# Performance work log

Hardware: AMD Instinct MI355X
Metric: run time of the kernel (lower is better)

Reference implementation:

```python
import jax, jax.numpy as jnp
import numpy as np

B, E, F_IN = 8192, 64, 7
D, H = 64, 4           # feature_size, heads
HD = D // H            # features per head


def setup_inputs() -> dict:
    key = jax.random.key(0)
    ks = jax.random.split(key, 14)
    def lin(k, i, o):
        return jax.random.normal(k, (i, o), jnp.float32) * (1.0 / np.sqrt(i))
    return {
        "x": jax.random.normal(ks[0], (B, E, F_IN), jnp.float32),
        # ego embedding MLP (7->64->64, with bias)
        "ego_w0": lin(ks[1], F_IN, D), "ego_b0": jnp.zeros((D,), jnp.float32),
        "ego_w1": lin(ks[2], D, D),    "ego_b1": jnp.zeros((D,), jnp.float32),
        # others embedding MLP (separate weights)
        "oth_w0": lin(ks[3], F_IN, D), "oth_b0": jnp.zeros((D,), jnp.float32),
        "oth_w1": lin(ks[4], D, D),    "oth_b1": jnp.zeros((D,), jnp.float32),
        # attention projections (no bias)
        "Wk": lin(ks[5], D, D), "Wv": lin(ks[6], D, D),
        "Wq": lin(ks[7], D, D), "Wc": lin(ks[8], D, D),
    }


def _mlp(x, w0, b0, w1, b1):
    h = jax.nn.relu(x @ w0 + b0)
    return jax.nn.relu(h @ w1 + b1)


def reference(x, ego_w0, ego_b0, ego_w1, ego_b1,
              oth_w0, oth_b0, oth_w1, oth_b1, Wk, Wv, Wq, Wc):
    b = x.shape[0]
    mask = x[:, :, 0] < 0.5                       # [B, E] absent entities
    ego = _mlp(x[:, 0:1, :], ego_w0, ego_b0, ego_w1, ego_b1)   # [B, 1, D]
    others = _mlp(x[:, 1:, :], oth_w0, oth_b0, oth_w1, oth_b1)  # [B, E-1, D]
    input_all = jnp.concatenate([ego, others], axis=1)          # [B, E, D]

    # project and split heads -> [B, H, E, HD]
    k = (input_all @ Wk).reshape(b, E, H, HD).transpose(0, 2, 1, 3)
    v = (input_all @ Wv).reshape(b, E, H, HD).transpose(0, 2, 1, 3)
    q = (ego @ Wq).reshape(b, 1, H, HD).transpose(0, 2, 1, 3)   # [B, H, 1, HD]

    scores = jnp.einsum('bhqd,bhkd->bhqk', q, k) / np.sqrt(HD)  # [B, H, 1, E]
    scores = jnp.where(mask[:, None, None, :], -1e9, scores)
    p_attn = jax.nn.softmax(scores, axis=-1)
    out = jnp.einsum('bhqk,bhkd->bhqd', p_attn, v)              # [B, H, 1, HD]
    out = out.reshape(b, D)                                      # concat heads
    result = (out @ Wc + ego[:, 0, :]) * 0.5                     # [B, D]
    return result
```

## Files before the change

### kernel.cpp

```cpp
#include <hip/hip_runtime.h>
#include <hip/hip_bf16.h>


typedef __attribute__((ext_vector_type(8))) short short8;
typedef __attribute__((ext_vector_type(4))) short short4b;
typedef __attribute__((ext_vector_type(4))) float f32x4;

#define SY 72

#define LDS_FENCE() asm volatile("s_waitcnt lgkmcnt(0)" ::: "memory")

#define WS_G    0
#define WS_EGW0 16384
#define WS_EGW1 16896
#define WS_WVT  20992
#define WS_WCT  25088
#define WS_W0T  29184
#define WS_W1T  29696

__device__ __forceinline__ short f2bs(float x) {
    __hip_bfloat16 h = __float2bfloat16(x);
    return __builtin_bit_cast(short, h);
}
__device__ __forceinline__ unsigned short f2u(float x) {
    __hip_bfloat16 h = __float2bfloat16(x);
    return __builtin_bit_cast(unsigned short, h);
}
__device__ __forceinline__ short8 ldws8(const unsigned short* p) {
    return *(const short8*)p;
}

__global__ void pack_ws(const float* __restrict__ ego_w0, const float* __restrict__ ego_w1,
                        const float* __restrict__ oth_w0, const float* __restrict__ oth_w1,
                        const float* __restrict__ Wk, const float* __restrict__ Wv,
                        const float* __restrict__ Wq, const float* __restrict__ Wc,
                        unsigned short* __restrict__ ws) {
    const int blk = blockIdx.x, t = threadIdx.x;
    if (blk < 256) {
        const int n = blk, h = n >> 6, f = n & 63, j = t;
        float a = 0.f;
#pragma unroll
        for (int d = 0; d < 16; ++d)
            a = fmaf(Wq[j * 64 + h * 16 + d], Wk[f * 64 + h * 16 + d], a);
        ws[WS_G + n * 64 + j] = f2u(a);
    } else {
        const int n = blk - 256, k = t;
        ws[WS_EGW1 + n * 64 + k] = f2u(ego_w1[k * 64 + n]);
        ws[WS_WVT  + n * 64 + k] = f2u(Wv[k * 64 + n]);
        ws[WS_WCT  + n * 64 + k] = f2u(Wc[k * 64 + n]);
        ws[WS_W1T  + n * 64 + k] = f2u(oth_w1[k * 64 + n]);
        if (k < 8) {
            ws[WS_EGW0 + n * 8 + k] = (k < 7) ? f2u(ego_w0[k * 64 + n]) : 0;
            ws[WS_W0T  + n * 8 + k] = (k < 7) ? f2u(oth_w0[k * 64 + n]) : 0;
        }
    }
}

__global__ __launch_bounds__(64, 2)
void ego_attn_kernel(const float* __restrict__ x,
                     const float* __restrict__ ego_b0, const float* __restrict__ ego_b1,
                     const float* __restrict__ oth_b0, const float* __restrict__ oth_b1,
                     const unsigned short* __restrict__ ws,
                     float* __restrict__ out)
{
    __shared__ __align__(16) short hy[64 * SY];
    __shared__ __align__(16) short chainbuf[4 * SY];
    __shared__ __align__(16) short kqb[16 * SY];
    __shared__ __align__(16) short pa[16 * SY];
    __shared__ __align__(16) short py[16 * SY];
    __shared__ __align__(16) short ob[4 * SY];
    __shared__ __align__(16) float mbuf[4][64];

    const int lane = threadIdx.x;
    const int lg = lane >> 4, ln = lane & 15;
    const int gb = blockIdx.x * 4;

    const short8 z8 = {0, 0, 0, 0, 0, 0, 0, 0};

    short8 w0f[4], w1f[2][4];
#pragma unroll
    for (int ct = 0; ct < 4; ++ct)
        w0f[ct] = (lg == 0) ? ldws8(ws + WS_W0T + (ct * 16 + ln) * 8) : z8;
#pragma unroll
    for (int kc = 0; kc < 2; ++kc)
#pragma unroll
        for (int ct = 0; ct < 4; ++ct)
            w1f[kc][ct] = ldws8(ws + WS_W1T + (ct * 16 + ln) * 64 + kc * 32 + lg * 8);
    float b0v[4], b1v[4], eb0v[4], eb1v[4];
#pragma unroll
    for (int ct = 0; ct < 4; ++ct) {
        b0v[ct]  = oth_b0[ct * 16 + ln];
        b1v[ct]  = oth_b1[ct * 16 + ln];
        eb0v[ct] = ego_b0[ct * 16 + ln];
        eb1v[ct] = ego_b1[ct * 16 + ln];
    }

    short8 xab[4][4];
#pragma unroll
    for (int i = 0; i < 4; ++i) {
        const float* xb = x + (size_t)(gb + i) * 448;
        mbuf[i][lane] = xb[lane * 7];
#pragma unroll
        for (int mt = 0; mt < 4; ++mt) {
            short8 v = z8;
            if (lg == 0) {
                const float* xr = xb + (mt * 16 + ln) * 7;
#pragma unroll
                for (int k = 0; k < 7; ++k) v[k] = f2bs(xr[k]);
            }
            xab[i][mt] = v;
        }
    }

    short8 xea = z8;
    if (lg == 0 && ln < 4) {
        const float* xr = x + (size_t)(gb + ln) * 448;
#pragma unroll
        for (int i = 0; i < 7; ++i) xea[i] = f2bs(xr[i]);
    }
#pragma unroll
    for (int ct = 0; ct < 4; ++ct) {
        const short8 bfr = (lg == 0) ? ldws8(ws + WS_EGW0 + (ct * 16 + ln) * 8) : z8;
        f32x4 c = {eb0v[ct], eb0v[ct], eb0v[ct], eb0v[ct]};
        c = __builtin_amdgcn_mfma_f32_16x16x32_bf16(xea, bfr, c, 0, 0, 0);
        if (lg == 0) {
#pragma unroll
            for (int r = 0; r < 4; ++r)
                chainbuf[r * SY + ct * 16 + ln] = f2bs(fmaxf(c[r], 0.f));
        }
    }
    LDS_FENCE();
    short8 ha[2];
#pragma unroll
    for (int kc = 0; kc < 2; ++kc)
        ha[kc] = *(const short8*)&chainbuf[(ln & 3) * SY + kc * 32 + lg * 8];
    LDS_FENCE();

    float egoR[4][4];
#pragma unroll
    for (int ct = 0; ct < 4; ++ct) {
        f32x4 c = {eb1v[ct], eb1v[ct], eb1v[ct], eb1v[ct]};
#pragma unroll
        for (int kc = 0; kc < 2; ++kc) {
            const short8 bfr = ldws8(ws + WS_EGW1 + (ct * 16 + ln) * 64 + kc * 32 + lg * 8);
            c = __builtin_amdgcn_mfma_f32_16x16x32_bf16(ha[kc], bfr, c, 0, 0, 0);
        }
#pragma unroll
        for (int r = 0; r < 4; ++r) egoR[ct][r] = fmaxf(c[r], 0.f);
    }
    if (lg == 0) {
#pragma unroll
        for (int ct = 0; ct < 4; ++ct)
#pragma unroll
            for (int r = 0; r < 4; ++r)
                chainbuf[r * SY + ct * 16 + ln] = f2bs(egoR[ct][r]);
    }
    LDS_FENCE();
    short8 ea[2];
#pragma unroll
    for (int kc = 0; kc < 2; ++kc)
        ea[kc] = *(const short8*)&chainbuf[(ln & 3) * SY + kc * 32 + lg * 8];

#pragma unroll
    for (int ctg = 0; ctg < 16; ++ctg) {
        f32x4 c = {0.f, 0.f, 0.f, 0.f};
#pragma unroll
        for (int kc = 0; kc < 2; ++kc) {
            const short8 bfr = ldws8(ws + WS_G + (ctg * 16 + ln) * 64 + kc * 32 + lg * 8);
            c = __builtin_amdgcn_mfma_f32_16x16x32_bf16(ea[kc], bfr, c, 0, 0, 0);
        }
        if (lg == 0) {
            const int h = ctg >> 2, fc = (ctg & 3) * 16 + ln;
#pragma unroll
            for (int r = 0; r < 4; ++r)
                kqb[(r * 4 + h) * SY + fc] = f2bs(c[r] * 0.25f);
        }
    }
    LDS_FENCE();

#pragma unroll
    for (int i = 0; i < 4; ++i) {
#pragma unroll
        for (int mt = 0; mt < 4; ++mt)
#pragma unroll
            for (int ct = 0; ct < 4; ++ct) {
                f32x4 c = {b0v[ct], b0v[ct], b0v[ct], b0v[ct]};
                c = __builtin_amdgcn_mfma_f32_16x16x32_bf16(xab[i][mt], w0f[ct], c, 0, 0, 0);
#pragma unroll
                for (int r = 0; r < 4; ++r)
                    hy[(mt * 16 + lg * 4 + r) * SY + ct * 16 + ln] = f2bs(fmaxf(c[r], 0.f));
            }
        LDS_FENCE();
        short8 a2[4][2];
#pragma unroll
        for (int mt = 0; mt < 4; ++mt)
#pragma unroll
            for (int kc = 0; kc < 2; ++kc)
                a2[mt][kc] = *(const short8*)&hy[(mt * 16 + ln) * SY + kc * 32 + lg * 8];
        LDS_FENCE();
#pragma unroll
        for (int ct = 0; ct < 4; ++ct)
#pragma unroll
            for (int mt = 0; mt < 4; ++mt) {
                f32x4 c = {b1v[ct], b1v[ct], b1v[ct], b1v[ct]};
                c = __builtin_amdgcn_mfma_f32_16x16x32_bf16(a2[mt][0], w1f[0][ct], c, 0, 0, 0);
                c = __builtin_amdgcn_mfma_f32_16x16x32_bf16(a2[mt][1], w1f[1][ct], c, 0, 0, 0);
#pragma unroll
                for (int r = 0; r < 4; ++r)
                    hy[(mt * 16 + lg * 4 + r) * SY + ct * 16 + ln] = f2bs(fmaxf(c[r], 0.f));
            }
        if (lg == 0) {
#pragma unroll
            for (int ct = 0; ct < 4; ++ct)
                hy[ct * 16 + ln] = f2bs(egoR[ct][i]);
        }
        LDS_FENCE();
        short8 ya[4][2];
#pragma unroll
        for (int mt = 0; mt < 4; ++mt)
#pragma unroll
            for (int kc = 0; kc < 2; ++kc)
                ya[mt][kc] = *(const short8*)&hy[(mt * 16 + ln) * SY + kc * 32 + lg * 8];
        short8 kb[2];
#pragma unroll
        for (int kc = 0; kc < 2; ++kc)
            kb[kc] = *(const short8*)&kqb[(i * 4 + (ln & 3)) * SY + kc * 32 + lg * 8];

        float sv[16];
        float m = -3e38f;
#pragma unroll
        for (int mt = 0; mt < 4; ++mt) {
            f32x4 c = {0.f, 0.f, 0.f, 0.f};
            c = __builtin_amdgcn_mfma_f32_16x16x32_bf16(ya[mt][0], kb[0], c, 0, 0, 0);
            c = __builtin_amdgcn_mfma_f32_16x16x32_bf16(ya[mt][1], kb[1], c, 0, 0, 0);
            const float4 mk = *(const float4*)&mbuf[i][mt * 16 + lg * 4];
            const float mkv[4] = {mk.x, mk.y, mk.z, mk.w};
#pragma unroll
            for (int r = 0; r < 4; ++r) {
                float s = c[r];
                if (mkv[r] < 0.5f) s = -1e9f;
                sv[mt * 4 + r] = s;
                m = fmaxf(m, s);
            }
        }
        m = fmaxf(m, __shfl_xor(m, 16));
        m = fmaxf(m, __shfl_xor(m, 32));
        float sum = 0.f;
#pragma unroll
        for (int k = 0; k < 16; ++k) { sv[k] = __expf(sv[k] - m); sum += sv[k]; }
        sum += __shfl_xor(sum, 16);
        sum += __shfl_xor(sum, 32);
        const float inv = 1.f / sum;
#pragma unroll
        for (int mt = 0; mt < 4; ++mt) {
            short4b pk;
#pragma unroll
            for (int r = 0; r < 4; ++r) pk[r] = f2bs(sv[mt * 4 + r] * inv);
            *(short4b*)&pa[ln * SY + mt * 16 + lg * 4] = pk;
        }
        LDS_FENCE();
        short8 pf[2];
#pragma unroll
        for (int kc = 0; kc < 2; ++kc)
            pf[kc] = *(const short8*)&pa[ln * SY + kc * 32 + lg * 8];
#pragma unroll
        for (int ct = 0; ct < 4; ++ct) {
            f32x4 c = {0.f, 0.f, 0.f, 0.f};
#pragma unroll
            for (int kc = 0; kc < 2; ++kc) {
                short8 yv;
#pragma unroll
                for (int j = 0; j < 8; ++j)
                    yv[j] = hy[(kc * 32 + lg * 8 + j) * SY + ct * 16 + ln];
                c = __builtin_amdgcn_mfma_f32_16x16x32_bf16(pf[kc], yv, c, 0, 0, 0);
            }
            if (lg == 0) {
#pragma unroll
                for (int r = 0; r < 4; ++r)
                    py[(r * 4 + i) * SY + ct * 16 + ln] = f2bs(c[r]);
            }
        }
        LDS_FENCE();
    }

#pragma unroll
    for (int ct = 0; ct < 4; ++ct) {
        short8 af[2];
#pragma unroll
        for (int kc = 0; kc < 2; ++kc)
            af[kc] = *(const short8*)&py[(ct * 4 + (ln & 3)) * SY + kc * 32 + lg * 8];
        f32x4 c = {0.f, 0.f, 0.f, 0.f};
#pragma unroll
        for (int kc = 0; kc < 2; ++kc) {
            const short8 bfr = ldws8(ws + WS_WVT + (ct * 16 + ln) * 64 + kc * 32 + lg * 8);
            c = __builtin_amdgcn_mfma_f32_16x16x32_bf16(af[kc], bfr, c, 0, 0, 0);
        }
        if (lg == 0) {
#pragma unroll
            for (int r = 0; r < 4; ++r)
                ob[r * SY + ct * 16 + ln] = f2bs(c[r]);
        }
    }
    LDS_FENCE();
    short8 oa[2];
#pragma unroll
    for (int kc = 0; kc < 2; ++kc)
        oa[kc] = *(const short8*)&ob[(ln & 3) * SY + kc * 32 + lg * 8];
#pragma unroll
    for (int ct = 0; ct < 4; ++ct) {
        f32x4 c = {0.f, 0.f, 0.f, 0.f};
#pragma unroll
        for (int kc = 0; kc < 2; ++kc) {
            const short8 bfr = ldws8(ws + WS_WCT + (ct * 16 + ln) * 64 + kc * 32 + lg * 8);
            c = __builtin_amdgcn_mfma_f32_16x16x32_bf16(oa[kc], bfr, c, 0, 0, 0);
        }
        if (lg == 0) {
#pragma unroll
            for (int r = 0; r < 4; ++r)
                out[(size_t)(gb + r) * 64 + ct * 16 + ln] = (c[r] + egoR[ct][r]) * 0.5f;
        }
    }
}

extern "C" void kernel_launch(void* const* d_in, const int* in_sizes, int n_in,
                              void* d_out, int out_size, void* d_ws, size_t ws_size,
                              hipStream_t stream) {
    const float* x      = (const float*)d_in[0];
    const float* ego_w0 = (const float*)d_in[1];
    const float* ego_b0 = (const float*)d_in[2];
    const float* ego_w1 = (const float*)d_in[3];
    const float* ego_b1 = (const float*)d_in[4];
    const float* oth_w0 = (const float*)d_in[5];
    const float* oth_b0 = (const float*)d_in[6];
    const float* oth_w1 = (const float*)d_in[7];
    const float* oth_b1 = (const float*)d_in[8];
    const float* Wk     = (const float*)d_in[9];
    const float* Wv     = (const float*)d_in[10];
    const float* Wq     = (const float*)d_in[11];
    const float* Wc     = (const float*)d_in[12];

    unsigned short* ws = (unsigned short*)d_ws;
    pack_ws<<<320, 64, 0, stream>>>(ego_w0, ego_w1, oth_w0, oth_w1,
                                    Wk, Wv, Wq, Wc, ws);
    ego_attn_kernel<<<2048, 64, 0, stream>>>(
        x, ego_b0, ego_b1, oth_b0, oth_b1, ws, (float*)d_out);
}
```

Before: 122.6 us.

## Halve batch rows per block, shrink LDS and registers to raise occupancy

Each 64-thread block now handles 2 batch rows instead of 4, so the grid doubles to 4096 blocks and launch bounds ask for 4 waves per SIMD. LDS buffers shrink (fewer rows, unpadded stride, chain and output buffers merged), and register-held fragment arrays are replaced by loads from LDS just before use, to cut VGPR pressure. The mask is now kept as per-lane bitmasks in registers instead of an LDS float buffer. In exchange, the 16-row MFMA tiles for the ego and attention steps are less used, and each block repeats weight-fragment loads for half as much work.

```diff
diff --git a/kernel.cpp b/kernel.cpp
--- a/kernel.cpp
+++ b/kernel.cpp
@@ -7,6 +7,7 @@
 typedef __attribute__((ext_vector_type(4))) float f32x4;
 
 #define SY 72
+#define SK 64
 
 #define LDS_FENCE() asm volatile("s_waitcnt lgkmcnt(0)" ::: "memory")
 
@@ -56,7 +57,7 @@
     }
 }
 
-__global__ __launch_bounds__(64, 2)
+__global__ __launch_bounds__(64, 4)
 void ego_attn_kernel(const float* __restrict__ x,
                      const float* __restrict__ ego_b0, const float* __restrict__ ego_b1,
                      const float* __restrict__ oth_b0, const float* __restrict__ oth_b1,
@@ -64,16 +65,14 @@
                      float* __restrict__ out)
 {
     __shared__ __align__(16) short hy[64 * SY];
-    __shared__ __align__(16) short chainbuf[4 * SY];
-    __shared__ __align__(16) short kqb[16 * SY];
-    __shared__ __align__(16) short pa[16 * SY];
-    __shared__ __align__(16) short py[16 * SY];
-    __shared__ __align__(16) short ob[4 * SY];
-    __shared__ __align__(16) float mbuf[4][64];
+    __shared__ __align__(16) short kqb[8 * SK];
+    __shared__ __align__(16) short pa[4 * SK];
+    __shared__ __align__(16) short py[8 * SK];
+    __shared__ __align__(16) short cbob[2 * SK];
 
     const int lane = threadIdx.x;
     const int lg = lane >> 4, ln = lane & 15;
-    const int gb = blockIdx.x * 4;
+    const int gb = blockIdx.x * 2;
 
     const short8 z8 = {0, 0, 0, 0, 0, 0, 0, 0};
 
@@ -95,11 +94,12 @@
         eb1v[ct] = ego_b1[ct * 16 + ln];
     }
 
-    short8 xab[4][4];
-#pragma unroll
-    for (int i = 0; i < 4; ++i) {
+    short8 xab[2][4];
+    unsigned mbits[2];
+#pragma unroll
+    for (int i = 0; i < 2; ++i) {
         const float* xb = x + (size_t)(gb + i) * 448;
-        mbuf[i][lane] = xb[lane * 7];
+        unsigned mb = 0;
 #pragma unroll
         for (int mt = 0; mt < 4; ++mt) {
             short8 v = z8;
@@ -109,14 +109,20 @@
                 for (int k = 0; k < 7; ++k) v[k] = f2bs(xr[k]);
             }
             xab[i][mt] = v;
-        }
+#pragma unroll
+            for (int r = 0; r < 4; ++r) {
+                const float mv = xb[(mt * 16 + lg * 4 + r) * 7];
+                if (mv < 0.5f) mb |= 1u << (mt * 4 + r);
+            }
+        }
+        mbits[i] = mb;
     }
 
     short8 xea = z8;
-    if (lg == 0 && ln < 4) {
+    if (lg == 0 && ln < 2) {
         const float* xr = x + (size_t)(gb + ln) * 448;
 #pragma unroll
-        for (int i = 0; i < 7; ++i) xea[i] = f2bs(xr[i]);
+        for (int k = 0; k < 7; ++k) xea[k] = f2bs(xr[k]);
     }
 #pragma unroll
     for (int ct = 0; ct < 4; ++ct) {
@@ -125,18 +131,18 @@
         c = __builtin_amdgcn_mfma_f32_16x16x32_bf16(xea, bfr, c, 0, 0, 0);
         if (lg == 0) {
 #pragma unroll
-            for (int r = 0; r < 4; ++r)
-                chainbuf[r * SY + ct * 16 + ln] = f2bs(fmaxf(c[r], 0.f));
+            for (int r = 0; r < 2; ++r)
+                cbob[r * SK + ct * 16 + ln] = f2bs(fmaxf(c[r], 0.f));
         }
     }
     LDS_FENCE();
     short8 ha[2];
 #pragma unroll
     for (int kc = 0; kc < 2; ++kc)
-        ha[kc] = *(const short8*)&chainbuf[(ln & 3) * SY + kc * 32 + lg * 8];
-    LDS_FENCE();
-
-    float egoR[4][4];
+        ha[kc] = *(const short8*)&cbob[(ln & 1) * SK + kc * 32 + lg * 8];
+    LDS_FENCE();
+
+    float egoR[4][2];
 #pragma unroll
     for (int ct = 0; ct < 4; ++ct) {
         f32x4 c = {eb1v[ct], eb1v[ct], eb1v[ct], eb1v[ct]};
@@ -146,20 +152,20 @@
             c = __builtin_amdgcn_mfma_f32_16x16x32_bf16(ha[kc], bfr, c, 0, 0, 0);
         }
 #pragma unroll
-        for (int r = 0; r < 4; ++r) egoR[ct][r] = fmaxf(c[r], 0.f);
+        for (int r = 0; r < 2; ++r) egoR[ct][r] = fmaxf(c[r], 0.f);
     }
     if (lg == 0) {
 #pragma unroll
         for (int ct = 0; ct < 4; ++ct)
 #pragma unroll
-            for (int r = 0; r < 4; ++r)
-                chainbuf[r * SY + ct * 16 + ln] = f2bs(egoR[ct][r]);
+            for (int r = 0; r < 2; ++r)
+                cbob[r * SK + ct * 16 + ln] = f2bs(egoR[ct][r]);
     }
     LDS_FENCE();
     short8 ea[2];
 #pragma unroll
     for (int kc = 0; kc < 2; ++kc)
-        ea[kc] = *(const short8*)&chainbuf[(ln & 3) * SY + kc * 32 + lg * 8];
+        ea[kc] = *(const short8*)&cbob[(ln & 1) * SK + kc * 32 + lg * 8];
 
 #pragma unroll
     for (int ctg = 0; ctg < 16; ++ctg) {
@@ -172,14 +178,14 @@
         if (lg == 0) {
             const int h = ctg >> 2, fc = (ctg & 3) * 16 + ln;
 #pragma unroll
-            for (int r = 0; r < 4; ++r)
-                kqb[(r * 4 + h) * SY + fc] = f2bs(c[r] * 0.25f);
-        }
-    }
-    LDS_FENCE();
-
-#pragma unroll
-    for (int i = 0; i < 4; ++i) {
+            for (int r = 0; r < 2; ++r)
+                kqb[(r * 4 + h) * SK + fc] = f2bs(c[r] * 0.25f);
+        }
+    }
+    LDS_FENCE();
+
+#pragma unroll
+    for (int i = 0; i < 2; ++i) {
 #pragma unroll
         for (int mt = 0; mt < 4; ++mt)
 #pragma unroll
@@ -191,54 +197,44 @@
                     hy[(mt * 16 + lg * 4 + r) * SY + ct * 16 + ln] = f2bs(fmaxf(c[r], 0.f));
             }
         LDS_FENCE();
-        short8 a2[4][2];
-#pragma unroll
-        for (int mt = 0; mt < 4; ++mt)
-#pragma unroll
-            for (int kc = 0; kc < 2; ++kc)
-                a2[mt][kc] = *(const short8*)&hy[(mt * 16 + ln) * SY + kc * 32 + lg * 8];
-        LDS_FENCE();
-#pragma unroll
-        for (int ct = 0; ct < 4; ++ct)
-#pragma unroll
-            for (int mt = 0; mt < 4; ++mt) {
+#pragma unroll
+        for (int mt = 0; mt < 4; ++mt) {
+            short8 a20 = *(const short8*)&hy[(mt * 16 + ln) * SY + 0 * 32 + lg * 8];
+            short8 a21 = *(const short8*)&hy[(mt * 16 + ln) * SY + 1 * 32 + lg * 8];
+#pragma unroll
+            for (int ct = 0; ct < 4; ++ct) {
                 f32x4 c = {b1v[ct], b1v[ct], b1v[ct], b1v[ct]};
-                c = __builtin_amdgcn_mfma_f32_16x16x32_bf16(a2[mt][0], w1f[0][ct], c, 0, 0, 0);
-                c = __builtin_amdgcn_mfma_f32_16x16x32_bf16(a2[mt][1], w1f[1][ct], c, 0, 0, 0);
+                c = __builtin_amdgcn_mfma_f32_16x16x32_bf16(a20, w1f[0][ct], c, 0, 0, 0);
+                c = __builtin_amdgcn_mfma_f32_16x16x32_bf16(a21, w1f[1][ct], c, 0, 0, 0);
 #pragma unroll
                 for (int r = 0; r < 4; ++r)
                     hy[(mt * 16 + lg * 4 + r) * SY + ct * 16 + ln] = f2bs(fmaxf(c[r], 0.f));
             }
+        }
         if (lg == 0) {
 #pragma unroll
             for (int ct = 0; ct < 4; ++ct)
                 hy[ct * 16 + ln] = f2bs(egoR[ct][i]);
         }
         LDS_FENCE();
-        short8 ya[4][2];
-#pragma unroll
-        for (int mt = 0; mt < 4; ++mt)
-#pragma unroll
-            for (int kc = 0; kc < 2; ++kc)
-                ya[mt][kc] = *(const short8*)&hy[(mt * 16 + ln) * SY + kc * 32 + lg * 8];
         short8 kb[2];
 #pragma unroll
         for (int kc = 0; kc < 2; ++kc)
-            kb[kc] = *(const short8*)&kqb[(i * 4 + (ln & 3)) * SY + kc * 32 + lg * 8];
+            kb[kc] = *(const short8*)&kqb[(i * 4 + (ln & 3)) * SK + kc * 32 + lg * 8];
 
         float sv[16];
         float m = -3e38f;
 #pragma unroll
         for (int mt = 0; mt < 4; ++mt) {
+            const short8 ya0 = *(const short8*)&hy[(mt * 16 + ln) * SY + 0 * 32 + lg * 8];
+            const short8 ya1 = *(const short8*)&hy[(mt * 16 + ln) * SY + 1 * 32 + lg * 8];
             f32x4 c = {0.f, 0.f, 0.f, 0.f};
-            c = __builtin_amdgcn_mfma_f32_16x16x32_bf16(ya[mt][0], kb[0], c, 0, 0, 0);
-            c = __builtin_amdgcn_mfma_f32_16x16x32_bf16(ya[mt][1], kb[1], c, 0, 0, 0);
-            const float4 mk = *(const float4*)&mbuf[i][mt * 16 + lg * 4];
-            const float mkv[4] = {mk.x, mk.y, mk.z, mk.w};
+            c = __builtin_amdgcn_mfma_f32_16x16x32_bf16(ya0, kb[0], c, 0, 0, 0);
+            c = __builtin_amdgcn_mfma_f32_16x16x32_bf16(ya1, kb[1], c, 0, 0, 0);
 #pragma unroll
             for (int r = 0; r < 4; ++r) {
                 float s = c[r];
-                if (mkv[r] < 0.5f) s = -1e9f;
+                if ((mbits[i] >> (mt * 4 + r)) & 1u) s = -1e9f;
                 sv[mt * 4 + r] = s;
                 m = fmaxf(m, s);
             }
@@ -251,18 +247,20 @@
         sum += __shfl_xor(sum, 16);
         sum += __shfl_xor(sum, 32);
         const float inv = 1.f / sum;
-#pragma unroll
-        for (int mt = 0; mt < 4; ++mt) {
-            short4b pk;
-#pragma unroll
-            for (int r = 0; r < 4; ++r) pk[r] = f2bs(sv[mt * 4 + r] * inv);
-            *(short4b*)&pa[ln * SY + mt * 16 + lg * 4] = pk;
+        if (ln < 4) {
+#pragma unroll
+            for (int mt = 0; mt < 4; ++mt) {
+                short4b pk;
+#pragma unroll
+                for (int r = 0; r < 4; ++r) pk[r] = f2bs(sv[mt * 4 + r] * inv);
+                *(short4b*)&pa[ln * SK + mt * 16 + lg * 4] = pk;
+            }
         }
         LDS_FENCE();
         short8 pf[2];
 #pragma unroll
         for (int kc = 0; kc < 2; ++kc)
-            pf[kc] = *(const short8*)&pa[ln * SY + kc * 32 + lg * 8];
+            pf[kc] = *(const short8*)&pa[(ln & 3) * SK + kc * 32 + lg * 8];
 #pragma unroll
         for (int ct = 0; ct < 4; ++ct) {
             f32x4 c = {0.f, 0.f, 0.f, 0.f};
@@ -277,7 +275,7 @@
             if (lg == 0) {
 #pragma unroll
                 for (int r = 0; r < 4; ++r)
-                    py[(r * 4 + i) * SY + ct * 16 + ln] = f2bs(c[r]);
+                    py[(r * 2 + i) * SK + ct * 16 + ln] = f2bs(c[r]);
             }
         }
         LDS_FENCE();
@@ -288,7 +286,7 @@
         short8 af[2];
 #pragma unroll
         for (int kc = 0; kc < 2; ++kc)
-            af[kc] = *(const short8*)&py[(ct * 4 + (ln & 3)) * SY + kc * 32 + lg * 8];
+            af[kc] = *(const short8*)&py[(ct * 2 + (ln & 1)) * SK + kc * 32 + lg * 8];
         f32x4 c = {0.f, 0.f, 0.f, 0.f};
 #pragma unroll
         for (int kc = 0; kc < 2; ++kc) {
@@ -297,15 +295,15 @@
         }
         if (lg == 0) {
 #pragma unroll
-            for (int r = 0; r < 4; ++r)
-                ob[r * SY + ct * 16 + ln] = f2bs(c[r]);
+            for (int r = 0; r < 2; ++r)
+                cbob[r * SK + ct * 16 + ln] = f2bs(c[r]);
         }
     }
     LDS_FENCE();
     short8 oa[2];
 #pragma unroll
     for (int kc = 0; kc < 2; ++kc)
-        oa[kc] = *(const short8*)&ob[(ln & 3) * SY + kc * 32 + lg * 8];
+        oa[kc] = *(const short8*)&cbob[(ln & 1) * SK + kc * 32 + lg * 8];
 #pragma unroll
     for (int ct = 0; ct < 4; ++ct) {
         f32x4 c = {0.f, 0.f, 0.f, 0.f};
@@ -316,7 +314,7 @@
         }
         if (lg == 0) {
 #pragma unroll
-            for (int r = 0; r < 4; ++r)
+            for (int r = 0; r < 2; ++r)
                 out[(size_t)(gb + r) * 64 + ct * 16 + ln] = (c[r] + egoR[ct][r]) * 0.5f;
         }
     }
@@ -342,6 +340,6 @@
     unsigned short* ws = (unsigned short*)d_ws;
     pack_ws<<<320, 64, 0, stream>>>(ego_w0, ego_w1, oth_w0, oth_w1,
                                     Wk, Wv, Wq, Wc, ws);
-    ego_attn_kernel<<<2048, 64, 0, stream>>>(
+    ego_attn_kernel<<<4096, 64, 0, stream>>>(
         x, ego_b0, ego_b1, oth_b0, oth_b1, ws, (float*)d_out);
 }
```

Result: slower. 181.5 us (+48.0%).

## Swap MFMA operand order for vector LDS stores and XOR-swizzle buffers

Applied to the files above, without the earlier changes.

Swaps the MFMA A/B operands so each lane holds four consecutive output columns. This lets results go to LDS as packed 4-short stores, and the Y buffers use an XOR swizzle in place of padded rows to avoid bank conflicts. A transposed copy of the second MLP layer output (yt) is computed with extra MFMAs, so the P·Y product can read contiguous short8 vectors instead of eight strided scalar loads. The mask is held as a 64-bit ballot instead of an LDS float buffer. In exchange it issues a second set of layer-2 MFMAs and uses more LDS.

```diff
diff --git a/kernel.cpp b/kernel.cpp
--- a/kernel.cpp
+++ b/kernel.cpp
@@ -5,8 +5,6 @@
 typedef __attribute__((ext_vector_type(8))) short short8;
 typedef __attribute__((ext_vector_type(4))) short short4b;
 typedef __attribute__((ext_vector_type(4))) float f32x4;
-
-#define SY 72
 
 #define LDS_FENCE() asm volatile("s_waitcnt lgkmcnt(0)" ::: "memory")
 
@@ -28,6 +26,18 @@
 }
 __device__ __forceinline__ short8 ldws8(const unsigned short* p) {
     return *(const short8*)p;
+}
+__device__ __forceinline__ short4b pk4r(f32x4 c) {
+    short4b p;
+#pragma unroll
+    for (int r = 0; r < 4; ++r) p[r] = f2bs(fmaxf(c[r], 0.f));
+    return p;
+}
+__device__ __forceinline__ short4b pk4(f32x4 c) {
+    short4b p;
+#pragma unroll
+    for (int r = 0; r < 4; ++r) p[r] = f2bs(c[r]);
+    return p;
 }
 
 __global__ void pack_ws(const float* __restrict__ ego_w0, const float* __restrict__ ego_w1,
@@ -63,43 +73,39 @@
                      const unsigned short* __restrict__ ws,
                      float* __restrict__ out)
 {
-    __shared__ __align__(16) short hy[64 * SY];
-    __shared__ __align__(16) short chainbuf[4 * SY];
-    __shared__ __align__(16) short kqb[16 * SY];
-    __shared__ __align__(16) short pa[16 * SY];
-    __shared__ __align__(16) short py[16 * SY];
-    __shared__ __align__(16) short ob[4 * SY];
-    __shared__ __align__(16) float mbuf[4][64];
+    __shared__ __align__(16) short hy[4096];
+    __shared__ __align__(16) short yt[4096];
+    __shared__ __align__(16) short kqb[1024];
+    __shared__ __align__(16) short pyb[1024];
+    __shared__ __align__(16) short s4[256];
 
     const int lane = threadIdx.x;
     const int lg = lane >> 4, ln = lane & 15;
     const int gb = blockIdx.x * 4;
-
     const short8 z8 = {0, 0, 0, 0, 0, 0, 0, 0};
 
     short8 w0f[4], w1f[2][4];
 #pragma unroll
-    for (int ct = 0; ct < 4; ++ct)
-        w0f[ct] = (lg == 0) ? ldws8(ws + WS_W0T + (ct * 16 + ln) * 8) : z8;
+    for (int t = 0; t < 4; ++t)
+        w0f[t] = (lg == 0) ? ldws8(ws + WS_W0T + (t * 16 + ln) * 8) : z8;
 #pragma unroll
     for (int kc = 0; kc < 2; ++kc)
 #pragma unroll
-        for (int ct = 0; ct < 4; ++ct)
-            w1f[kc][ct] = ldws8(ws + WS_W1T + (ct * 16 + ln) * 64 + kc * 32 + lg * 8);
-    float b0v[4], b1v[4], eb0v[4], eb1v[4];
-#pragma unroll
-    for (int ct = 0; ct < 4; ++ct) {
-        b0v[ct]  = oth_b0[ct * 16 + ln];
-        b1v[ct]  = oth_b1[ct * 16 + ln];
-        eb0v[ct] = ego_b0[ct * 16 + ln];
-        eb1v[ct] = ego_b1[ct * 16 + ln];
+        for (int t = 0; t < 4; ++t)
+            w1f[kc][t] = ldws8(ws + WS_W1T + (t * 16 + ln) * 64 + kc * 32 + lg * 8);
+    float b1v[4], eb1v[4];
+#pragma unroll
+    for (int t = 0; t < 4; ++t) {
+        b1v[t]  = oth_b1[t * 16 + ln];
+        eb1v[t] = ego_b1[t * 16 + ln];
     }
 
     short8 xab[4][4];
+    unsigned long long mb64[4];
 #pragma unroll
     for (int i = 0; i < 4; ++i) {
         const float* xb = x + (size_t)(gb + i) * 448;
-        mbuf[i][lane] = xb[lane * 7];
+        mb64[i] = __ballot(xb[lane * 7] < 0.5f);
 #pragma unroll
         for (int mt = 0; mt < 4; ++mt) {
             short8 v = z8;
@@ -111,39 +117,36 @@
             xab[i][mt] = v;
         }
     }
-
     short8 xea = z8;
     if (lg == 0 && ln < 4) {
         const float* xr = x + (size_t)(gb + ln) * 448;
 #pragma unroll
-        for (int i = 0; i < 7; ++i) xea[i] = f2bs(xr[i]);
-    }
-#pragma unroll
-    for (int ct = 0; ct < 4; ++ct) {
-        const short8 bfr = (lg == 0) ? ldws8(ws + WS_EGW0 + (ct * 16 + ln) * 8) : z8;
-        f32x4 c = {eb0v[ct], eb0v[ct], eb0v[ct], eb0v[ct]};
-        c = __builtin_amdgcn_mfma_f32_16x16x32_bf16(xea, bfr, c, 0, 0, 0);
-        if (lg == 0) {
-#pragma unroll
-            for (int r = 0; r < 4; ++r)
-                chainbuf[r * SY + ct * 16 + ln] = f2bs(fmaxf(c[r], 0.f));
-        }
+        for (int k = 0; k < 7; ++k) xea[k] = f2bs(xr[k]);
+    }
+
+#pragma unroll
+    for (int dt = 0; dt < 4; ++dt) {
+        const short8 af = (lg == 0) ? ldws8(ws + WS_EGW0 + (dt * 16 + ln) * 8) : z8;
+        const float4 bq = *(const float4*)&ego_b0[dt * 16 + lg * 4];
+        f32x4 c = {bq.x, bq.y, bq.z, bq.w};
+        c = __builtin_amdgcn_mfma_f32_16x16x32_bf16(af, xea, c, 0, 0, 0);
+        if (ln < 4)
+            *(short4b*)&s4[ln * 64 + dt * 16 + lg * 4] = pk4r(c);
     }
     LDS_FENCE();
     short8 ha[2];
 #pragma unroll
     for (int kc = 0; kc < 2; ++kc)
-        ha[kc] = *(const short8*)&chainbuf[(ln & 3) * SY + kc * 32 + lg * 8];
-    LDS_FENCE();
-
+        ha[kc] = *(const short8*)&s4[(ln & 3) * 64 + kc * 32 + lg * 8];
+    LDS_FENCE();
     float egoR[4][4];
 #pragma unroll
     for (int ct = 0; ct < 4; ++ct) {
         f32x4 c = {eb1v[ct], eb1v[ct], eb1v[ct], eb1v[ct]};
 #pragma unroll
         for (int kc = 0; kc < 2; ++kc) {
-            const short8 bfr = ldws8(ws + WS_EGW1 + (ct * 16 + ln) * 64 + kc * 32 + lg * 8);
-            c = __builtin_amdgcn_mfma_f32_16x16x32_bf16(ha[kc], bfr, c, 0, 0, 0);
+            const short8 b = ldws8(ws + WS_EGW1 + (ct * 16 + ln) * 64 + kc * 32 + lg * 8);
+            c = __builtin_amdgcn_mfma_f32_16x16x32_bf16(ha[kc], b, c, 0, 0, 0);
         }
 #pragma unroll
         for (int r = 0; r < 4; ++r) egoR[ct][r] = fmaxf(c[r], 0.f);
@@ -153,27 +156,26 @@
         for (int ct = 0; ct < 4; ++ct)
 #pragma unroll
             for (int r = 0; r < 4; ++r)
-                chainbuf[r * SY + ct * 16 + ln] = f2bs(egoR[ct][r]);
+                s4[r * 64 + ct * 16 + ln] = f2bs(egoR[ct][r]);
     }
     LDS_FENCE();
     short8 ea[2];
 #pragma unroll
     for (int kc = 0; kc < 2; ++kc)
-        ea[kc] = *(const short8*)&chainbuf[(ln & 3) * SY + kc * 32 + lg * 8];
-
+        ea[kc] = *(const short8*)&s4[(ln & 3) * 64 + kc * 32 + lg * 8];
 #pragma unroll
     for (int ctg = 0; ctg < 16; ++ctg) {
         f32x4 c = {0.f, 0.f, 0.f, 0.f};
 #pragma unroll
         for (int kc = 0; kc < 2; ++kc) {
-            const short8 bfr = ldws8(ws + WS_G + (ctg * 16 + ln) * 64 + kc * 32 + lg * 8);
-            c = __builtin_amdgcn_mfma_f32_16x16x32_bf16(ea[kc], bfr, c, 0, 0, 0);
-        }
-        if (lg == 0) {
-            const int h = ctg >> 2, fc = (ctg & 3) * 16 + ln;
-#pragma unroll
-            for (int r = 0; r < 4; ++r)
-                kqb[(r * 4 + h) * SY + fc] = f2bs(c[r] * 0.25f);
+            const short8 g = ldws8(ws + WS_G + (ctg * 16 + ln) * 64 + kc * 32 + lg * 8);
+            c = __builtin_amdgcn_mfma_f32_16x16x32_bf16(g, ea[kc], c, 0, 0, 0);
+        }
+        if (ln < 4) {
+            f32x4 cs;
+#pragma unroll
+            for (int r = 0; r < 4; ++r) cs[r] = c[r] * 0.25f;
+            *(short4b*)&kqb[(ln * 4 + (ctg >> 2)) * 64 + (ctg & 3) * 16 + lg * 4] = pk4(cs);
         }
     }
     LDS_FENCE();
@@ -181,64 +183,73 @@
 #pragma unroll
     for (int i = 0; i < 4; ++i) {
 #pragma unroll
+        for (int dt = 0; dt < 4; ++dt) {
+            const float4 bq = *(const float4*)&oth_b0[dt * 16 + lg * 4];
+#pragma unroll
+            for (int et = 0; et < 4; ++et) {
+                f32x4 c = {bq.x, bq.y, bq.z, bq.w};
+                c = __builtin_amdgcn_mfma_f32_16x16x32_bf16(w0f[dt], xab[i][et], c, 0, 0, 0);
+                *(short4b*)&hy[(et * 16 + ln) * 64 +
+                               ((((dt * 2 + (lg >> 1)) ^ (ln & 7)) << 3) | ((lg & 1) << 2))] = pk4r(c);
+            }
+        }
+        LDS_FENCE();
+        short8 a2[4][2];
+#pragma unroll
         for (int mt = 0; mt < 4; ++mt)
 #pragma unroll
+            for (int kc = 0; kc < 2; ++kc)
+                a2[mt][kc] = *(const short8*)&hy[(mt * 16 + ln) * 64 +
+                                                 (((kc * 4 + lg) ^ (ln & 7)) << 3)];
+        LDS_FENCE();
+#pragma unroll
+        for (int mt = 0; mt < 4; ++mt)
+#pragma unroll
             for (int ct = 0; ct < 4; ++ct) {
-                f32x4 c = {b0v[ct], b0v[ct], b0v[ct], b0v[ct]};
-                c = __builtin_amdgcn_mfma_f32_16x16x32_bf16(xab[i][mt], w0f[ct], c, 0, 0, 0);
-#pragma unroll
-                for (int r = 0; r < 4; ++r)
-                    hy[(mt * 16 + lg * 4 + r) * SY + ct * 16 + ln] = f2bs(fmaxf(c[r], 0.f));
-            }
-        LDS_FENCE();
-        short8 a2[4][2];
-#pragma unroll
-        for (int mt = 0; mt < 4; ++mt)
-#pragma unroll
-            for (int kc = 0; kc < 2; ++kc)
-                a2[mt][kc] = *(const short8*)&hy[(mt * 16 + ln) * SY + kc * 32 + lg * 8];
-        LDS_FENCE();
-#pragma unroll
-        for (int ct = 0; ct < 4; ++ct)
-#pragma unroll
-            for (int mt = 0; mt < 4; ++mt) {
                 f32x4 c = {b1v[ct], b1v[ct], b1v[ct], b1v[ct]};
                 c = __builtin_amdgcn_mfma_f32_16x16x32_bf16(a2[mt][0], w1f[0][ct], c, 0, 0, 0);
                 c = __builtin_amdgcn_mfma_f32_16x16x32_bf16(a2[mt][1], w1f[1][ct], c, 0, 0, 0);
-#pragma unroll
-                for (int r = 0; r < 4; ++r)
-                    hy[(mt * 16 + lg * 4 + r) * SY + ct * 16 + ln] = f2bs(fmaxf(c[r], 0.f));
-            }
+                *(short4b*)&yt[(ct * 16 + ln) * 64 +
+                               ((((mt * 2 + (lg >> 1)) ^ (ln & 7)) << 3) | ((lg & 1) << 2))] = pk4r(c);
+            }
+#pragma unroll
+        for (int dt = 0; dt < 4; ++dt) {
+            const float4 bq = *(const float4*)&oth_b1[dt * 16 + lg * 4];
+#pragma unroll
+            for (int et = 0; et < 4; ++et) {
+                f32x4 c = {bq.x, bq.y, bq.z, bq.w};
+                c = __builtin_amdgcn_mfma_f32_16x16x32_bf16(w1f[0][dt], a2[et][0], c, 0, 0, 0);
+                c = __builtin_amdgcn_mfma_f32_16x16x32_bf16(w1f[1][dt], a2[et][1], c, 0, 0, 0);
+                *(short4b*)&hy[(et * 16 + ln) * 64 +
+                               ((((dt * 2 + (lg >> 1)) ^ (ln & 7)) << 3) | ((lg & 1) << 2))] = pk4r(c);
+            }
+        }
         if (lg == 0) {
 #pragma unroll
-            for (int ct = 0; ct < 4; ++ct)
-                hy[ct * 16 + ln] = f2bs(egoR[ct][i]);
-        }
-        LDS_FENCE();
-        short8 ya[4][2];
-#pragma unroll
-        for (int mt = 0; mt < 4; ++mt)
-#pragma unroll
-            for (int kc = 0; kc < 2; ++kc)
-                ya[mt][kc] = *(const short8*)&hy[(mt * 16 + ln) * SY + kc * 32 + lg * 8];
+            for (int ct = 0; ct < 4; ++ct) {
+                const short ev = f2bs(egoR[ct][i]);
+                hy[ct * 16 + ln] = ev;
+                yt[(ct * 16 + ln) * 64 + ((ln & 7) << 3)] = ev;
+            }
+        }
+        LDS_FENCE();
         short8 kb[2];
 #pragma unroll
         for (int kc = 0; kc < 2; ++kc)
-            kb[kc] = *(const short8*)&kqb[(i * 4 + (ln & 3)) * SY + kc * 32 + lg * 8];
-
+            kb[kc] = *(const short8*)&kqb[(i * 4 + (ln & 3)) * 64 + kc * 32 + lg * 8];
         float sv[16];
         float m = -3e38f;
 #pragma unroll
         for (int mt = 0; mt < 4; ++mt) {
+            const short8 ya0 = *(const short8*)&hy[(mt * 16 + ln) * 64 + (((lg) ^ (ln & 7)) << 3)];
+            const short8 ya1 = *(const short8*)&hy[(mt * 16 + ln) * 64 + (((4 + lg) ^ (ln & 7)) << 3)];
             f32x4 c = {0.f, 0.f, 0.f, 0.f};
-            c = __builtin_amdgcn_mfma_f32_16x16x32_bf16(ya[mt][0], kb[0], c, 0, 0, 0);
-            c = __builtin_amdgcn_mfma_f32_16x16x32_bf16(ya[mt][1], kb[1], c, 0, 0, 0);
-            const float4 mk = *(const float4*)&mbuf[i][mt * 16 + lg * 4];
-            const float mkv[4] = {mk.x, mk.y, mk.z, mk.w};
+            c = __builtin_amdgcn_mfma_f32_16x16x32_bf16(ya0, kb[0], c, 0, 0, 0);
+            c = __builtin_amdgcn_mfma_f32_16x16x32_bf16(ya1, kb[1], c, 0, 0, 0);
 #pragma unroll
             for (int r = 0; r < 4; ++r) {
                 float s = c[r];
-                if (mkv[r] < 0.5f) s = -1e9f;
+                if ((mb64[i] >> (mt * 16 + lg * 4 + r)) & 1ull) s = -1e9f;
                 sv[mt * 4 + r] = s;
                 m = fmaxf(m, s);
             }
@@ -251,33 +262,33 @@
         sum += __shfl_xor(sum, 16);
         sum += __shfl_xor(sum, 32);
         const float inv = 1.f / sum;
-#pragma unroll
-        for (int mt = 0; mt < 4; ++mt) {
-            short4b pk;
-#pragma unroll
-            for (int r = 0; r < 4; ++r) pk[r] = f2bs(sv[mt * 4 + r] * inv);
-            *(short4b*)&pa[ln * SY + mt * 16 + lg * 4] = pk;
+        if (ln < 4) {
+#pragma unroll
+            for (int mt = 0; mt < 4; ++mt) {
+                short4b pk;
+#pragma unroll
+                for (int r = 0; r < 4; ++r) pk[r] = f2bs(sv[mt * 4 + r] * inv);
+                *(short4b*)&s4[ln * 64 + mt * 16 + lg * 4] = pk;
+            }
         }
         LDS_FENCE();
         short8 pf[2];
 #pragma unroll
         for (int kc = 0; kc < 2; ++kc)
-            pf[kc] = *(const short8*)&pa[ln * SY + kc * 32 + lg * 8];
+            pf[kc] = *(const short8*)&s4[(ln & 3) * 64 + kc * 32 + lg * 8];
 #pragma unroll
         for (int ct = 0; ct < 4; ++ct) {
             f32x4 c = {0.f, 0.f, 0.f, 0.f};
 #pragma unroll
             for (int kc = 0; kc < 2; ++kc) {
-                short8 yv;
-#pragma unroll
-                for (int j = 0; j < 8; ++j)
-                    yv[j] = hy[(kc * 32 + lg * 8 + j) * SY + ct * 16 + ln];
+                const short8 yv = *(const short8*)&yt[(ct * 16 + ln) * 64 +
+                                                      (((kc * 4 + lg) ^ (ln & 7)) << 3)];
                 c = __builtin_amdgcn_mfma_f32_16x16x32_bf16(pf[kc], yv, c, 0, 0, 0);
             }
             if (lg == 0) {
 #pragma unroll
                 for (int r = 0; r < 4; ++r)
-                    py[(r * 4 + i) * SY + ct * 16 + ln] = f2bs(c[r]);
+                    pyb[(r * 4 + i) * 64 + ct * 16 + ln] = f2bs(c[r]);
             }
         }
         LDS_FENCE();
@@ -288,31 +299,31 @@
         short8 af[2];
 #pragma unroll
         for (int kc = 0; kc < 2; ++kc)
-            af[kc] = *(const short8*)&py[(ct * 4 + (ln & 3)) * SY + kc * 32 + lg * 8];
+            af[kc] = *(const short8*)&pyb[(ct * 4 + (ln & 3)) * 64 + kc * 32 + lg * 8];
         f32x4 c = {0.f, 0.f, 0.f, 0.f};
 #pragma unroll
         for (int kc = 0; kc < 2; ++kc) {
-            const short8 bfr = ldws8(ws + WS_WVT + (ct * 16 + ln) * 64 + kc * 32 + lg * 8);
-            c = __builtin_amdgcn_mfma_f32_16x16x32_bf16(af[kc], bfr, c, 0, 0, 0);
+            const short8 b = ldws8(ws + WS_WVT + (ct * 16 + ln) * 64 + kc * 32 + lg * 8);
+            c = __builtin_amdgcn_mfma_f32_16x16x32_bf16(af[kc], b, c, 0, 0, 0);
         }
         if (lg == 0) {
 #pragma unroll
             for (int r = 0; r < 4; ++r)
-                ob[r * SY + ct * 16 + ln] = f2bs(c[r]);
+                kqb[r * 64 + ct * 16 + ln] = f2bs(c[r]);
         }
     }
     LDS_FENCE();
     short8 oa[2];
 #pragma unroll
     for (int kc = 0; kc < 2; ++kc)
-        oa[kc] = *(const short8*)&ob[(ln & 3) * SY + kc * 32 + lg * 8];
+        oa[kc] = *(const short8*)&kqb[(ln & 3) * 64 + kc * 32 + lg * 8];
 #pragma unroll
     for (int ct = 0; ct < 4; ++ct) {
         f32x4 c = {0.f, 0.f, 0.f, 0.f};
 #pragma unroll
         for (int kc = 0; kc < 2; ++kc) {
-            const short8 bfr = ldws8(ws + WS_WCT + (ct * 16 + ln) * 64 + kc * 32 + lg * 8);
-            c = __builtin_amdgcn_mfma_f32_16x16x32_bf16(oa[kc], bfr, c, 0, 0, 0);
+            const short8 b = ldws8(ws + WS_WCT + (ct * 16 + ln) * 64 + kc * 32 + lg * 8);
+            c = __builtin_amdgcn_mfma_f32_16x16x32_bf16(oa[kc], b, c, 0, 0, 0);
         }
         if (lg == 0) {
 #pragma unroll
```

After: 141.0 us. 1.15x slower.

## Stage inputs and ego state in LDS to cut register pressure

Applied to the files above, without the earlier changes.

The bf16-converted entity features are no longer held in 64 registers per lane. They are written once to an LDS staging buffer and reloaded per batch item. The mask becomes a 64-bit ballot instead of an LDS float array, and the ego embedding moves to LDS instead of a 16-float register array. Intermediate buffers are folded into hy, and the main loop is no longer unrolled, all to shrink VGPR use and allow more waves per CU. The trade-off is extra LDS traffic and less instruction-level overlap from the rolled loop.

```diff
diff --git a/kernel.cpp b/kernel.cpp
--- a/kernel.cpp
+++ b/kernel.cpp
@@ -64,17 +64,16 @@
                      float* __restrict__ out)
 {
     __shared__ __align__(16) short hy[64 * SY];
-    __shared__ __align__(16) short chainbuf[4 * SY];
     __shared__ __align__(16) short kqb[16 * SY];
-    __shared__ __align__(16) short pa[16 * SY];
+    __shared__ __align__(16) short pa[4 * SY];
     __shared__ __align__(16) short py[16 * SY];
-    __shared__ __align__(16) short ob[4 * SY];
-    __shared__ __align__(16) float mbuf[4][64];
+    __shared__ __align__(16) short xld[4 * 64 * 8];
+    __shared__ __align__(16) float egf[4 * 64];
+    __shared__ unsigned long long mball[4];
 
     const int lane = threadIdx.x;
     const int lg = lane >> 4, ln = lane & 15;
     const int gb = blockIdx.x * 4;
-
     const short8 z8 = {0, 0, 0, 0, 0, 0, 0, 0};
 
     short8 w0f[4], w1f[2][4];
@@ -95,28 +94,25 @@
         eb1v[ct] = ego_b1[ct * 16 + ln];
     }
 
-    short8 xab[4][4];
 #pragma unroll
     for (int i = 0; i < 4; ++i) {
-        const float* xb = x + (size_t)(gb + i) * 448;
-        mbuf[i][lane] = xb[lane * 7];
-#pragma unroll
-        for (int mt = 0; mt < 4; ++mt) {
-            short8 v = z8;
-            if (lg == 0) {
-                const float* xr = xb + (mt * 16 + ln) * 7;
-#pragma unroll
-                for (int k = 0; k < 7; ++k) v[k] = f2bs(xr[k]);
-            }
-            xab[i][mt] = v;
-        }
-    }
-
-    short8 xea = z8;
-    if (lg == 0 && ln < 4) {
-        const float* xr = x + (size_t)(gb + ln) * 448;
-#pragma unroll
-        for (int i = 0; i < 7; ++i) xea[i] = f2bs(xr[i]);
+        const float* xr = x + (size_t)(gb + i) * 448 + lane * 7;
+        const float v0 = xr[0];
+        const unsigned long long mb = __ballot(v0 < 0.5f);
+        if (lane == 0) mball[i] = mb;
+        short8 v;
+        v[0] = f2bs(v0);
+#pragma unroll
+        for (int k = 1; k < 7; ++k) v[k] = f2bs(xr[k]);
+        v[7] = 0;
+        *(short8*)&xld[((i << 6) | lane) * 8] = v;
+    }
+    LDS_FENCE();
+
+    short8 xea;
+    {
+        const short8 t = *(const short8*)&xld[((ln & 3) << 6) * 8];
+        xea = (lg == 0 && ln < 4) ? t : z8;
     }
 #pragma unroll
     for (int ct = 0; ct < 4; ++ct) {
@@ -126,17 +122,15 @@
         if (lg == 0) {
 #pragma unroll
             for (int r = 0; r < 4; ++r)
-                chainbuf[r * SY + ct * 16 + ln] = f2bs(fmaxf(c[r], 0.f));
+                hy[r * SY + ct * 16 + ln] = f2bs(fmaxf(c[r], 0.f));
         }
     }
     LDS_FENCE();
     short8 ha[2];
 #pragma unroll
     for (int kc = 0; kc < 2; ++kc)
-        ha[kc] = *(const short8*)&chainbuf[(ln & 3) * SY + kc * 32 + lg * 8];
-    LDS_FENCE();
-
-    float egoR[4][4];
+        ha[kc] = *(const short8*)&hy[(ln & 3) * SY + kc * 32 + lg * 8];
+    LDS_FENCE();
 #pragma unroll
     for (int ct = 0; ct < 4; ++ct) {
         f32x4 c = {eb1v[ct], eb1v[ct], eb1v[ct], eb1v[ct]};
@@ -145,23 +139,22 @@
             const short8 bfr = ldws8(ws + WS_EGW1 + (ct * 16 + ln) * 64 + kc * 32 + lg * 8);
             c = __builtin_amdgcn_mfma_f32_16x16x32_bf16(ha[kc], bfr, c, 0, 0, 0);
         }
-#pragma unroll
-        for (int r = 0; r < 4; ++r) egoR[ct][r] = fmaxf(c[r], 0.f);
-    }
-    if (lg == 0) {
-#pragma unroll
-        for (int ct = 0; ct < 4; ++ct)
-#pragma unroll
-            for (int r = 0; r < 4; ++r)
-                chainbuf[r * SY + ct * 16 + ln] = f2bs(egoR[ct][r]);
+        if (lg == 0) {
+#pragma unroll
+            for (int r = 0; r < 4; ++r) {
+                const float e = fmaxf(c[r], 0.f);
+                egf[r * 64 + ct * 16 + ln] = e;
+                hy[r * SY + ct * 16 + ln] = f2bs(e);
+            }
+        }
     }
     LDS_FENCE();
     short8 ea[2];
 #pragma unroll
     for (int kc = 0; kc < 2; ++kc)
-        ea[kc] = *(const short8*)&chainbuf[(ln & 3) * SY + kc * 32 + lg * 8];
-
-#pragma unroll
+        ea[kc] = *(const short8*)&hy[(ln & 3) * SY + kc * 32 + lg * 8];
+
+#pragma unroll 4
     for (int ctg = 0; ctg < 16; ++ctg) {
         f32x4 c = {0.f, 0.f, 0.f, 0.f};
 #pragma unroll
@@ -178,14 +171,22 @@
     }
     LDS_FENCE();
 
-#pragma unroll
+#pragma unroll 1
     for (int i = 0; i < 4; ++i) {
+        short8 xa[4];
+#pragma unroll
+        for (int mt = 0; mt < 4; ++mt) {
+            const short8 t = *(const short8*)&xld[((i << 6) | (mt * 16 + ln)) * 8];
+            xa[mt] = (lg == 0) ? t : z8;
+        }
+        const unsigned long long mb = mball[i];
+
 #pragma unroll
         for (int mt = 0; mt < 4; ++mt)
 #pragma unroll
             for (int ct = 0; ct < 4; ++ct) {
                 f32x4 c = {b0v[ct], b0v[ct], b0v[ct], b0v[ct]};
-                c = __builtin_amdgcn_mfma_f32_16x16x32_bf16(xab[i][mt], w0f[ct], c, 0, 0, 0);
+                c = __builtin_amdgcn_mfma_f32_16x16x32_bf16(xa[mt], w0f[ct], c, 0, 0, 0);
 #pragma unroll
                 for (int r = 0; r < 4; ++r)
                     hy[(mt * 16 + lg * 4 + r) * SY + ct * 16 + ln] = f2bs(fmaxf(c[r], 0.f));
@@ -212,15 +213,9 @@
         if (lg == 0) {
 #pragma unroll
             for (int ct = 0; ct < 4; ++ct)
-                hy[ct * 16 + ln] = f2bs(egoR[ct][i]);
-        }
-        LDS_FENCE();
-        short8 ya[4][2];
-#pragma unroll
-        for (int mt = 0; mt < 4; ++mt)
-#pragma unroll
-            for (int kc = 0; kc < 2; ++kc)
-                ya[mt][kc] = *(const short8*)&hy[(mt * 16 + ln) * SY + kc * 32 + lg * 8];
+                hy[ct * 16 + ln] = f2bs(egf[i * 64 + ct * 16 + ln]);
+        }
+        LDS_FENCE();
         short8 kb[2];
 #pragma unroll
         for (int kc = 0; kc < 2; ++kc)
@@ -230,15 +225,15 @@
         float m = -3e38f;
 #pragma unroll
         for (int mt = 0; mt < 4; ++mt) {
+            const short8 ya0 = *(const short8*)&hy[(mt * 16 + ln) * SY + 0 * 32 + lg * 8];
+            const short8 ya1 = *(const short8*)&hy[(mt * 16 + ln) * SY + 1 * 32 + lg * 8];
             f32x4 c = {0.f, 0.f, 0.f, 0.f};
-            c = __builtin_amdgcn_mfma_f32_16x16x32_bf16(ya[mt][0], kb[0], c, 0, 0, 0);
-            c = __builtin_amdgcn_mfma_f32_16x16x32_bf16(ya[mt][1], kb[1], c, 0, 0, 0);
-            const float4 mk = *(const float4*)&mbuf[i][mt * 16 + lg * 4];
-            const float mkv[4] = {mk.x, mk.y, mk.z, mk.w};
+            c = __builtin_amdgcn_mfma_f32_16x16x32_bf16(ya0, kb[0], c, 0, 0, 0);
+            c = __builtin_amdgcn_mfma_f32_16x16x32_bf16(ya1, kb[1], c, 0, 0, 0);
 #pragma unroll
             for (int r = 0; r < 4; ++r) {
                 float s = c[r];
-                if (mkv[r] < 0.5f) s = -1e9f;
+                if ((mb >> (mt * 16 + lg * 4 + r)) & 1ull) s = -1e9f;
                 sv[mt * 4 + r] = s;
                 m = fmaxf(m, s);
             }
@@ -251,18 +246,20 @@
         sum += __shfl_xor(sum, 16);
         sum += __shfl_xor(sum, 32);
         const float inv = 1.f / sum;
-#pragma unroll
-        for (int mt = 0; mt < 4; ++mt) {
-            short4b pk;
-#pragma unroll
-            for (int r = 0; r < 4; ++r) pk[r] = f2bs(sv[mt * 4 + r] * inv);
-            *(short4b*)&pa[ln * SY + mt * 16 + lg * 4] = pk;
+        if (ln < 4) {
+#pragma unroll
+            for (int mt = 0; mt < 4; ++mt) {
+                short4b pk;
+#pragma unroll
+                for (int r = 0; r < 4; ++r) pk[r] = f2bs(sv[mt * 4 + r] * inv);
+                *(short4b*)&pa[ln * SY + mt * 16 + lg * 4] = pk;
+            }
         }
         LDS_FENCE();
         short8 pf[2];
 #pragma unroll
         for (int kc = 0; kc < 2; ++kc)
-            pf[kc] = *(const short8*)&pa[ln * SY + kc * 32 + lg * 8];
+            pf[kc] = *(const short8*)&pa[(ln & 3) * SY + kc * 32 + lg * 8];
 #pragma unroll
         for (int ct = 0; ct < 4; ++ct) {
             f32x4 c = {0.f, 0.f, 0.f, 0.f};
@@ -298,14 +295,14 @@
         if (lg == 0) {
 #pragma unroll
             for (int r = 0; r < 4; ++r)
-                ob[r * SY + ct * 16 + ln] = f2bs(c[r]);
+                hy[r * SY + ct * 16 + ln] = f2bs(c[r]);
         }
     }
     LDS_FENCE();
     short8 oa[2];
 #pragma unroll
     for (int kc = 0; kc < 2; ++kc)
-        oa[kc] = *(const short8*)&ob[(ln & 3) * SY + kc * 32 + lg * 8];
+        oa[kc] = *(const short8*)&hy[(ln & 3) * SY + kc * 32 + lg * 8];
 #pragma unroll
     for (int ct = 0; ct < 4; ++ct) {
         f32x4 c = {0.f, 0.f, 0.f, 0.f};
@@ -317,7 +314,7 @@
         if (lg == 0) {
 #pragma unroll
             for (int r = 0; r < 4; ++r)
-                out[(size_t)(gb + r) * 64 + ct * 16 + ln] = (c[r] + egoR[ct][r]) * 0.5f;
+                out[(size_t)(gb + r) * 64 + ct * 16 + ln] = (c[r] + egf[r * 64 + ct * 16 + ln]) * 0.5f;
         }
     }
 }
```

Result: no change. 121.5 us (-0.9%).
